# Performance work log

Hardware: AMD Instinct MI355X
Metric: run time of the kernel (lower is better)

Reference implementation:

```python
import jax, jax.numpy as jnp
import numpy as np

N_NODES = 8      # objects per graph (fixed in source)
N_AT = 16        # anchors/targets vocab: 8 colors + 8 markers
H = 128          # n_hidden
BS = 16384


def _mlp(x, W1, b1, W2, b2):
    # layers.fully_connected default activation is relu; second layer linear.
    # dropout is identity in eval mode.
    return jax.nn.relu(x @ W1 + b1) @ W2 + b2


def _edges_and_segments(bs):
    # static edge list: all ordered pairs (i,j), i != j, per graph, offset per batch
    ii, jj = np.meshgrid(np.arange(N_NODES), np.arange(N_NODES), indexing='ij')
    m = ii != jj
    base = np.stack([ii[m], jj[m]], axis=1)                      # [56, 2]
    offs = (np.arange(bs) * N_NODES)[:, None, None]
    edges = (base[None] + offs).reshape(-1, 2).astype(np.int32)  # [bs*56, 2]
    seg_ids = np.repeat(np.arange(bs), N_NODES).astype(np.int32) # [bs*8]
    return jnp.asarray(edges), jnp.asarray(seg_ids)


def setup_inputs() -> dict:
    key = jax.random.key(0)
    ks = jax.random.split(key, 14)

    anchors = jax.random.randint(ks[0], (BS,), 0, N_AT)
    n_jumps = jax.random.randint(ks[1], (BS,), 0, N_NODES)
    positions = jax.random.uniform(ks[2], (BS, N_NODES, 2), dtype=jnp.float32)
    colors = jax.random.randint(ks[3], (BS, N_NODES), 0, 8)
    markers = jax.random.randint(ks[4], (BS, N_NODES), 8, 16)  # markers live in [8,16)

    def lin(k, fan_in, fan_out):
        return jax.random.normal(k, (fan_in, fan_out), dtype=jnp.float32) / np.sqrt(fan_in)

    d_in = 2 + 8 + 8 + N_AT + N_NODES  # pos + color_oh + marker_oh + question(16+8) = 42
    z = lambda n: jnp.zeros((n,), jnp.float32)
    return {
        'anchors': anchors, 'n_jumps': n_jumps, 'positions': positions,
        'colors': colors, 'markers': markers,
        'pre_W1': lin(ks[5], d_in, H),     'pre_b1': z(H),
        'pre_W2': lin(ks[6], H, H),        'pre_b2': z(H),
        'msg_W1': lin(ks[7], 2 * H + 1, H),'msg_b1': z(H),
        'msg_W2': lin(ks[8], H, H),        'msg_b2': z(H),
        'post_W1': lin(ks[9], 2 * H, H),   'post_b1': z(H),
        'post_W2': lin(ks[10], H, H),      'post_b2': z(H),
        'out_W1': lin(ks[11], H, H),       'out_b1': z(H),
        'out_W2': lin(ks[12], H, N_AT),    'out_b2': z(N_AT),
    }


def reference(anchors, n_jumps, positions, colors, markers,
              pre_W1, pre_b1, pre_W2, pre_b2,
              msg_W1, msg_b1, msg_W2, msg_b2,
              post_W1, post_b1, post_W2, post_b2,
              out_W1, out_b1, out_W2, out_b2):
    bs = positions.shape[0]
    edges, seg_ids = _edges_and_segments(bs)
    n_total = bs * N_NODES

    col_oh = jax.nn.one_hot(colors, 8, dtype=jnp.float32).reshape(n_total, 8)
    mrk_oh = jax.nn.one_hot(markers - 8, 8, dtype=jnp.float32).reshape(n_total, 8)
    pos = positions.reshape(n_total, 2)

    # pairwise euclidean distance per edge -> [E, 1]
    dp = pos[edges[:, 0]] - pos[edges[:, 1]]
    dist = jnp.sqrt(jnp.sum(dp * dp, axis=1, keepdims=True))

    # question broadcast to every node of its graph
    q = jnp.concatenate([jax.nn.one_hot(anchors, N_AT, dtype=jnp.float32),
                         jax.nn.one_hot(n_jumps, N_NODES, dtype=jnp.float32)], axis=1)
    q = q[seg_ids]  # [bs*8, 24]

    x0 = _mlp(jnp.concatenate([pos, col_oh, mrk_oh, q], axis=1),
              pre_W1, pre_b1, pre_W2, pre_b2)  # [bs*8, H]

    # one message-passing step: gather -> MLP -> scatter(segment_sum on source idx)
    mi = jnp.concatenate([x0[edges[:, 0]], x0[edges[:, 1]], dist], axis=1)  # [E, 257]
    msgs = _mlp(mi, msg_W1, msg_b1, msg_W2, msg_b2)                          # [E, H]
    upd = jax.ops.segment_sum(msgs, edges[:, 0], num_segments=n_total)       # [bs*8, H]

    x = _mlp(jnp.concatenate([upd, x0], axis=1), post_W1, post_b1, post_W2, post_b2)

    logits = jax.ops.segment_sum(x, seg_ids, num_segments=bs)  # [bs, H]
    logits = _mlp(logits, out_W1, out_b1, out_W2, out_b2)      # [bs, 16]
    return logits
```

## Files before the change

kernel.cpp:

```cpp
#include <hip/hip_runtime.h>

#define LROW 136

typedef __bf16 bf16x8  __attribute__((ext_vector_type(8)));
typedef __bf16 bf16x4v __attribute__((ext_vector_type(4)));
typedef __bf16 bf16x2v __attribute__((ext_vector_type(2)));
typedef float  f32x4   __attribute__((ext_vector_type(4)));
typedef float  f32x2   __attribute__((ext_vector_type(2)));

#define MFMA16(a, b, c) __builtin_amdgcn_mfma_f32_16x16x32_bf16((a), (b), (c), 0, 0, 0)

__device__ __forceinline__ float bflo(unsigned v) { return __uint_as_float(v << 16); }
__device__ __forceinline__ float bfhi(unsigned v) { return __uint_as_float(v & 0xffff0000u); }

__device__ __forceinline__ unsigned short f2bf_u16(float f) {
  unsigned u = __float_as_uint(f);
  u += 0x7fffu + ((u >> 16) & 1u);
  return (unsigned short)(u >> 16);
}

__global__ void combine_weights(
    const float* __restrict__ pre_W2, const float* __restrict__ msg_W1,
    const float* __restrict__ msg_W2, const float* __restrict__ post_W1,
    const float* __restrict__ post_W2, const float* __restrict__ out_W1,
    const float* __restrict__ out_W2, const float* __restrict__ pre_b2,
    const float* __restrict__ msg_b1, const float* __restrict__ msg_b2,
    const float* __restrict__ post_b1, const float* __restrict__ post_b2,
    const float* __restrict__ out_b1,
    unsigned short* __restrict__ WabT, unsigned short* __restrict__ WdT,
    unsigned short* __restrict__ WcT, unsigned short* __restrict__ WoT,
    unsigned short* __restrict__ Wo2T, float* __restrict__ vecs)
{
  __shared__ float part[256];
  const int b = blockIdx.x;
  const int t = threadIdx.x;
  if (b < 320) {
    const int p  = b >> 6;
    const int kp = b & 63;
    const int k  = kp * 2 + (t >> 7);
    const int n  = t & 127;
    const float* L; const float* R; unsigned short* O;
    if (p == 0)      { L = pre_W2;  R = msg_W1;             O = WabT; }
    else if (p == 1) { L = pre_W2;  R = msg_W1 + 128*128;   O = WabT + 128*128; }
    else if (p == 2) { L = pre_W2;  R = post_W1 + 128*128;  O = WdT; }
    else if (p == 3) { L = msg_W2;  R = post_W1;            O = WcT; }
    else             { L = post_W2; R = out_W1;             O = WoT; }
    const float* Lr = L + k * 128;
    float a0 = 0.f, a1 = 0.f, a2 = 0.f, a3 = 0.f;
    #pragma unroll 8
    for (int m = 0; m < 128; m += 4) {
      a0 = fmaf(Lr[m + 0], R[(m + 0) * 128 + n], a0);
      a1 = fmaf(Lr[m + 1], R[(m + 1) * 128 + n], a1);
      a2 = fmaf(Lr[m + 2], R[(m + 2) * 128 + n], a2);
      a3 = fmaf(Lr[m + 3], R[(m + 3) * 128 + n], a3);
    }
    O[n * 128 + k] = f2bf_u16((a0 + a1) + (a2 + a3));
  } else if (b == 320) {
    for (int idx = t; idx < 16 * 128; idx += 256) {
      int o = idx >> 7, k = idx & 127;
      Wo2T[o * 128 + k] = f2bf_u16(out_W2[k * 16 + o]);
    }
    if (t < 128) vecs[t] = msg_W1[256 * 128 + t];
  } else {
    const int n = t & 127;
    const int h = t >> 7;
    float s = 0.f;
    if (b == 321) {
      #pragma unroll 8
      for (int m = h * 64; m < h * 64 + 64; ++m)
        s = fmaf(pre_b2[m], msg_W1[m * 128 + n] + msg_W1[(128 + m) * 128 + n], s);
    } else if (b == 322) {
      #pragma unroll 8
      for (int m = h * 64; m < h * 64 + 64; ++m) {
        s = fmaf(7.f * msg_b2[m], post_W1[m * 128 + n], s);
        s = fmaf(pre_b2[m], post_W1[(128 + m) * 128 + n], s);
      }
    } else {
      #pragma unroll 8
      for (int m = h * 64; m < h * 64 + 64; ++m)
        s = fmaf(8.f * post_b2[m], out_W1[m * 128 + n], s);
    }
    part[t] = s;
    __syncthreads();
    if (t < 128) {
      float r = part[t] + part[t + 128];
      if (b == 321)      vecs[128 + t] = r + msg_b1[t];
      else if (b == 322) vecs[256 + t] = r + post_b1[t];
      else               vecs[384 + t] = r + out_b1[t];
    }
  }
}

__global__ void __launch_bounds__(256, 4) rrn_main(
    const int* __restrict__ anchors, const int* __restrict__ n_jumps,
    const float* __restrict__ positions, const int* __restrict__ colors,
    const int* __restrict__ markers, const float* __restrict__ pre_W1,
    const float* __restrict__ pre_b1,
    const __bf16* __restrict__ WabT, const __bf16* __restrict__ WdT,
    const __bf16* __restrict__ WcT, const __bf16* __restrict__ WoT,
    const __bf16* __restrict__ Wo2T, const float* __restrict__ vecs,
    const float* __restrict__ out_b2, float* __restrict__ out)
{
  __shared__ __align__(16) char smem[38912];
  __bf16* Ab   = (__bf16*)(smem);
  float*  sW1s = (float*)(smem);
  float*  qrow = (float*)(smem + 9216);
  float*  posL = (float*)(smem + 13312);
  int*    cmk  = (int*)(smem + 13824);
  __bf16* h1   = (__bf16*)(smem + 17408);
  __bf16* Bb   = (__bf16*)(smem + 17408);
  __bf16* Sph  = (__bf16*)(smem + 17408);
  __bf16* hob  = (__bf16*)(smem + 21760);
  float*  dist = (float*)(smem + 34816);
  float*  vec  = (float*)(smem + 36864);

  const int tid  = threadIdx.x;
  const int lane = tid & 63;
  const int w    = tid >> 6;
  const int l15  = lane & 15;
  const int quad = lane >> 4;
  const int colw = w * 32;
  const int g0   = blockIdx.x * 8;
  const int n0   = blockIdx.x * 64;

  for (int i = tid; i < 18 * 128; i += 256) sW1s[i] = pre_W1[i];
  {
    const int n = tid & 127;
    for (int g = (tid >> 7); g < 8; g += 2) {
      int a = anchors[g0 + g], nj = n_jumps[g0 + g];
      qrow[g * 128 + n] = pre_b1[n] + pre_W1[(18 + a) * 128 + n]
                        + pre_W1[(34 + nj) * 128 + n];
    }
  }
  if (tid < 128) posL[tid] = positions[n0 * 2 + tid];
  else if (tid < 192) {
    int node = tid - 128;
    cmk[node] = colors[n0 + node] | ((markers[n0 + node] - 8) << 8);
  }
  for (int i = tid; i < 512; i += 256) {
    int g = i >> 6, ii = (i >> 3) & 7, jj = i & 7;
    const float* pa = positions + (n0 + g * 8 + ii) * 2;
    const float* pb = positions + (n0 + g * 8 + jj) * 2;
    float dx = pa[0] - pb[0], dy = pa[1] - pb[1];
    dist[i] = sqrtf(dx * dx + dy * dy);
  }
  for (int i = tid; i < 512; i += 256) vec[i] = vecs[i];
  __syncthreads();

  {
    const int p  = (tid & 63) * 2;
    const int rh = tid >> 6;
    const f32x2 z2 = {0.f, 0.f};
    const f32x2 wx = *(const f32x2*)&sW1s[p];
    const f32x2 wy = *(const f32x2*)&sW1s[128 + p];
    #pragma unroll 4
    for (int rr = 0; rr < 16; ++rr) {
      int r = rh * 16 + rr;
      float px = posL[r * 2], py = posL[r * 2 + 1];
      int cm = cmk[r];
      int c = cm & 255, mk = cm >> 8;
      f32x2 acc = *(const f32x2*)&qrow[(r >> 3) * 128 + p];
      acc += *(const f32x2*)&sW1s[(2 + c) * 128 + p];
      acc += *(const f32x2*)&sW1s[(10 + mk) * 128 + p];
      f32x2 px2 = {px, px}, py2 = {py, py};
      acc = __builtin_elementwise_fma(px2, wx, acc);
      acc = __builtin_elementwise_fma(py2, wy, acc);
      acc = __builtin_elementwise_max(acc, z2);
      bf16x2v o = { (__bf16)acc.x, (__bf16)acc.y };
      *(bf16x2v*)&h1[r * LROW + p] = o;
    }
  }
  __syncthreads();

  f32x4 acc1[4][4];
  {
    f32x4 zero = {0.f, 0.f, 0.f, 0.f};
    #pragma unroll
    for (int mt = 0; mt < 4; ++mt)
      #pragma unroll
      for (int nt = 0; nt < 4; ++nt) acc1[mt][nt] = zero;
  }
  #pragma unroll
  for (int kb = 0; kb < 128; kb += 32) {
    const int ko = kb + quad * 8;
    bf16x8 fa[4], fb[4];
    #pragma unroll
    for (int mt = 0; mt < 4; ++mt)
      fa[mt] = *(const bf16x8*)&h1[(mt * 16 + l15) * LROW + ko];
    fb[0] = *(const bf16x8*)&WabT[(colw + l15) * 128 + ko];
    fb[1] = *(const bf16x8*)&WabT[(colw + 16 + l15) * 128 + ko];
    fb[2] = *(const bf16x8*)&WabT[(128 + colw + l15) * 128 + ko];
    fb[3] = *(const bf16x8*)&WabT[(128 + colw + 16 + l15) * 128 + ko];
    #pragma unroll
    for (int mt = 0; mt < 4; ++mt)
      #pragma unroll
      for (int nt = 0; nt < 4; ++nt)
        acc1[mt][nt] = MFMA16(fa[mt], fb[nt], acc1[mt][nt]);
  }
  #pragma unroll
  for (int mt = 0; mt < 4; ++mt)
    #pragma unroll
    for (int nt = 0; nt < 2; ++nt) {
      int col = colw + nt * 16 + l15;
      #pragma unroll
      for (int r = 0; r < 4; ++r)
        Ab[(mt * 16 + quad * 4 + r) * LROW + col] = (__bf16)acc1[mt][nt][r];
    }

  f32x4 accD[4][2];
  {
    f32x4 zero = {0.f, 0.f, 0.f, 0.f};
    #pragma unroll
    for (int mt = 0; mt < 4; ++mt) { accD[mt][0] = zero; accD[mt][1] = zero; }
  }
  #pragma unroll
  for (int kb = 0; kb < 128; kb += 32) {
    const int ko = kb + quad * 8;
    bf16x8 fa[4], fd[2];
    #pragma unroll
    for (int mt = 0; mt < 4; ++mt)
      fa[mt] = *(const bf16x8*)&h1[(mt * 16 + l15) * LROW + ko];
    fd[0] = *(const bf16x8*)&WdT[(colw + l15) * 128 + ko];
    fd[1] = *(const bf16x8*)&WdT[(colw + 16 + l15) * 128 + ko];
    #pragma unroll
    for (int mt = 0; mt < 4; ++mt) {
      accD[mt][0] = MFMA16(fa[mt], fd[0], accD[mt][0]);
      accD[mt][1] = MFMA16(fa[mt], fd[1], accD[mt][1]);
    }
  }
  __syncthreads();
  #pragma unroll
  for (int mt = 0; mt < 4; ++mt)
    #pragma unroll
    for (int nt = 2; nt < 4; ++nt) {
      int col = colw + (nt - 2) * 16 + l15;
      #pragma unroll
      for (int r = 0; r < 4; ++r)
        Bb[(mt * 16 + quad * 4 + r) * LROW + col] = (__bf16)acc1[mt][nt][r];
    }
  __syncthreads();

  {
    const int g   = tid >> 5;
    const int nb4 = (tid & 31) * 4;
    const f32x2 w0 = *(const f32x2*)&vec[nb4];
    const f32x2 w1 = *(const f32x2*)&vec[nb4 + 2];
    const f32x2 c0 = *(const f32x2*)&vec[128 + nb4];
    const f32x2 c1 = *(const f32x2*)&vec[128 + nb4 + 2];
    const f32x2 z2 = {0.f, 0.f};
    f32x2 B0[8], B1[8];
    #pragma unroll
    for (int j = 0; j < 8; ++j) {
      uint2 vb = *(const uint2*)&Bb[(g * 8 + j) * LROW + nb4];
      B0[j].x = bflo(vb.x); B0[j].y = bfhi(vb.x);
      B1[j].x = bflo(vb.y); B1[j].y = bfhi(vb.y);
    }
    #pragma unroll
    for (int i = 0; i < 8; ++i) {
      uint2 va = *(const uint2*)&Ab[(g * 8 + i) * LROW + nb4];
      f32x2 a0; a0.x = bflo(va.x); a0.y = bfhi(va.x); a0 += c0;
      f32x2 a1; a1.x = bflo(va.y); a1.y = bfhi(va.y); a1 += c1;
      f32x2 s0 = z2, s1 = z2;
      #pragma unroll
      for (int j = 0; j < 8; ++j) {
        if (j == i) continue;
        float d = dist[g * 64 + i * 8 + j];
        f32x2 d2 = {d, d};
        f32x2 t0 = __builtin_elementwise_fma(d2, w0, B0[j]) + a0;
        f32x2 t1 = __builtin_elementwise_fma(d2, w1, B1[j]) + a1;
        t0 = __builtin_elementwise_max(t0, z2);
        t1 = __builtin_elementwise_max(t1, z2);
        s0 += t0; s1 += t1;
      }
      bf16x4v o = { (__bf16)s0.x, (__bf16)s0.y, (__bf16)s1.x, (__bf16)s1.y };
      *(bf16x4v*)&Ab[(g * 8 + i) * LROW + nb4] = o;
    }
  }
  __syncthreads();

  {
    const __bf16* Sb = Ab;
    #pragma unroll
    for (int kb = 0; kb < 128; kb += 32) {
      const int ko = kb + quad * 8;
      bf16x8 fa[4], fc[2];
      #pragma unroll
      for (int mt = 0; mt < 4; ++mt)
        fa[mt] = *(const bf16x8*)&Sb[(mt * 16 + l15) * LROW + ko];
      fc[0] = *(const bf16x8*)&WcT[(colw + l15) * 128 + ko];
      fc[1] = *(const bf16x8*)&WcT[(colw + 16 + l15) * 128 + ko];
      #pragma unroll
      for (int mt = 0; mt < 4; ++mt) {
        accD[mt][0] = MFMA16(fa[mt], fc[0], accD[mt][0]);
        accD[mt][1] = MFMA16(fa[mt], fc[1], accD[mt][1]);
      }
    }
    #pragma unroll
    for (int mt = 0; mt < 4; ++mt)
      #pragma unroll
      for (int dt = 0; dt < 2; ++dt) {
        int col = colw + dt * 16 + l15;
        float cp = vec[256 + col];
        f32x4 a = accD[mt][dt];
        float s = fmaxf(a[0] + cp, 0.f) + fmaxf(a[1] + cp, 0.f)
                + fmaxf(a[2] + cp, 0.f) + fmaxf(a[3] + cp, 0.f);
        s += __shfl_xor(s, 16);
        int grow = mt * 2 + (lane >= 32 ? 1 : 0);
        if ((lane & 31) < 16) Sph[grow * LROW + col] = (__bf16)s;
        else                  Sph[(8 + grow) * LROW + col] = (__bf16)0.f;
      }
  }
  __syncthreads();

  {
    f32x4 acco[2];
    f32x4 zero = {0.f, 0.f, 0.f, 0.f};
    acco[0] = zero; acco[1] = zero;
    #pragma unroll
    for (int kb = 0; kb < 128; kb += 32) {
      const int ko = kb + quad * 8;
      bf16x8 fa = *(const bf16x8*)&Sph[l15 * LROW + ko];
      bf16x8 fb0 = *(const bf16x8*)&WoT[(colw + l15) * 128 + ko];
      bf16x8 fb1 = *(const bf16x8*)&WoT[(colw + 16 + l15) * 128 + ko];
      acco[0] = MFMA16(fa, fb0, acco[0]);
      acco[1] = MFMA16(fa, fb1, acco[1]);
    }
    #pragma unroll
    for (int dt = 0; dt < 2; ++dt) {
      int col = colw + dt * 16 + l15;
      float co = vec[384 + col];
      #pragma unroll
      for (int r = 0; r < 4; ++r)
        hob[(quad * 4 + r) * LROW + col] = (__bf16)fmaxf(acco[dt][r] + co, 0.f);
    }
  }
  __syncthreads();

  if (w == 0) {
    f32x4 accf = {0.f, 0.f, 0.f, 0.f};
    #pragma unroll
    for (int kb = 0; kb < 128; kb += 32) {
      const int ko = kb + quad * 8;
      bf16x8 fa  = *(const bf16x8*)&hob[l15 * LROW + ko];
      bf16x8 fbv = *(const bf16x8*)&Wo2T[l15 * 128 + ko];
      accf = MFMA16(fa, fbv, accf);
    }
    if (quad < 2) {
      float b2 = out_b2[l15];
      #pragma unroll
      for (int r = 0; r < 4; ++r) {
        int row = quad * 4 + r;
        out[(g0 + row) * 16 + l15] = accf[r] + b2;
      }
    }
  }
}

extern "C" void kernel_launch(void* const* d_in, const int* in_sizes, int n_in,
                              void* d_out, int out_size, void* d_ws, size_t ws_size,
                              hipStream_t stream) {
  const int*   anchors   = (const int*)d_in[0];
  const int*   n_jumps   = (const int*)d_in[1];
  const float* positions = (const float*)d_in[2];
  const int*   colors    = (const int*)d_in[3];
  const int*   markers   = (const int*)d_in[4];
  const float* pre_W1  = (const float*)d_in[5];
  const float* pre_b1  = (const float*)d_in[6];
  const float* pre_W2  = (const float*)d_in[7];
  const float* pre_b2  = (const float*)d_in[8];
  const float* msg_W1  = (const float*)d_in[9];
  const float* msg_b1  = (const float*)d_in[10];
  const float* msg_W2  = (const float*)d_in[11];
  const float* msg_b2  = (const float*)d_in[12];
  const float* post_W1 = (const float*)d_in[13];
  const float* post_b1 = (const float*)d_in[14];
  const float* post_W2 = (const float*)d_in[15];
  const float* post_b2 = (const float*)d_in[16];
  const float* out_W1  = (const float*)d_in[17];
  const float* out_b1  = (const float*)d_in[18];
  const float* out_W2  = (const float*)d_in[19];
  const float* out_b2  = (const float*)d_in[20];

  char* ws = (char*)d_ws;
  unsigned short* WabT = (unsigned short*)(ws);
  unsigned short* WdT  = (unsigned short*)(ws + 65536);
  unsigned short* WcT  = (unsigned short*)(ws + 98304);
  unsigned short* WoT  = (unsigned short*)(ws + 131072);
  unsigned short* Wo2T = (unsigned short*)(ws + 163840);
  float*          vecs = (float*)(ws + 167936);

  const int BS = in_sizes[0];

  combine_weights<<<324, 256, 0, stream>>>(
      pre_W2, msg_W1, msg_W2, post_W1, post_W2, out_W1, out_W2,
      pre_b2, msg_b1, msg_b2, post_b1, post_b2, out_b1,
      WabT, WdT, WcT, WoT, Wo2T, vecs);

  rrn_main<<<BS / 8, 256, 0, stream>>>(
      anchors, n_jumps, positions, colors, markers, pre_W1, pre_b1,
      (const __bf16*)WabT, (const __bf16*)WdT, (const __bf16*)WcT,
      (const __bf16*)WoT, (const __bf16*)Wo2T, vecs, out_b2, (float*)d_out);
}
```

Baseline: 156.0 us.

## Halve graphs per block and shrink shared memory to raise occupancy

```diff
diff --git a/kernel.cpp b/kernel.cpp
--- a/kernel.cpp
+++ b/kernel.cpp
@@ -91,7 +91,7 @@
   }
 }
 
-__global__ void __launch_bounds__(256, 4) rrn_main(
+__global__ void __launch_bounds__(256, 6) rrn_main(
     const int* __restrict__ anchors, const int* __restrict__ n_jumps,
     const float* __restrict__ positions, const int* __restrict__ colors,
     const int* __restrict__ markers, const float* __restrict__ pre_W1,
@@ -101,18 +101,18 @@
     const __bf16* __restrict__ Wo2T, const float* __restrict__ vecs,
     const float* __restrict__ out_b2, float* __restrict__ out)
 {
-  __shared__ __align__(16) char smem[38912];
-  __bf16* Ab   = (__bf16*)(smem);
-  float*  sW1s = (float*)(smem);
-  float*  qrow = (float*)(smem + 9216);
-  float*  posL = (float*)(smem + 13312);
-  int*    cmk  = (int*)(smem + 13824);
-  __bf16* h1   = (__bf16*)(smem + 17408);
-  __bf16* Bb   = (__bf16*)(smem + 17408);
-  __bf16* Sph  = (__bf16*)(smem + 17408);
-  __bf16* hob  = (__bf16*)(smem + 21760);
-  float*  dist = (float*)(smem + 34816);
-  float*  vec  = (float*)(smem + 36864);
+  __shared__ __align__(16) char smem[20480];
+  float*  vec  = (float*)(smem);
+  float*  dist = (float*)(smem + 2048);
+  __bf16* Ab   = (__bf16*)(smem + 3072);
+  __bf16* sW1b = (__bf16*)(smem + 3072);
+  float*  qrow = (float*)(smem + 7680);
+  float*  posL = (float*)(smem + 9728);
+  short*  cmk  = (short*)(smem + 9984);
+  __bf16* h1   = (__bf16*)(smem + 11776);
+  __bf16* Bb   = (__bf16*)(smem + 11776);
+  __bf16* Sph  = (__bf16*)(smem + 11776);
+  __bf16* hob  = (__bf16*)(smem + 16128);
 
   const int tid  = threadIdx.x;
   const int lane = tid & 63;
@@ -120,48 +120,51 @@
   const int l15  = lane & 15;
   const int quad = lane >> 4;
   const int colw = w * 32;
-  const int g0   = blockIdx.x * 8;
-  const int n0   = blockIdx.x * 64;
-
-  for (int i = tid; i < 18 * 128; i += 256) sW1s[i] = pre_W1[i];
+  const int g0   = blockIdx.x * 4;
+  const int n0   = blockIdx.x * 32;
+
+  for (int i = tid; i < 18 * 128; i += 256) sW1b[i] = (__bf16)pre_W1[i];
   {
     const int n = tid & 127;
-    for (int g = (tid >> 7); g < 8; g += 2) {
+    for (int g = (tid >> 7); g < 4; g += 2) {
       int a = anchors[g0 + g], nj = n_jumps[g0 + g];
       qrow[g * 128 + n] = pre_b1[n] + pre_W1[(18 + a) * 128 + n]
                         + pre_W1[(34 + nj) * 128 + n];
     }
   }
-  if (tid < 128) posL[tid] = positions[n0 * 2 + tid];
-  else if (tid < 192) {
-    int node = tid - 128;
-    cmk[node] = colors[n0 + node] | ((markers[n0 + node] - 8) << 8);
-  }
-  for (int i = tid; i < 512; i += 256) {
-    int g = i >> 6, ii = (i >> 3) & 7, jj = i & 7;
+  if (tid < 64) posL[tid] = positions[n0 * 2 + tid];
+  else if (tid < 96) {
+    int node = tid - 64;
+    cmk[node] = (short)(colors[n0 + node] | ((markers[n0 + node] - 8) << 8));
+  }
+  {
+    int g = tid >> 6, ii = (tid >> 3) & 7, jj = tid & 7;
     const float* pa = positions + (n0 + g * 8 + ii) * 2;
     const float* pb = positions + (n0 + g * 8 + jj) * 2;
     float dx = pa[0] - pb[0], dy = pa[1] - pb[1];
-    dist[i] = sqrtf(dx * dx + dy * dy);
+    dist[tid] = sqrtf(dx * dx + dy * dy);
   }
   for (int i = tid; i < 512; i += 256) vec[i] = vecs[i];
   __syncthreads();
 
   {
-    const int p  = (tid & 63) * 2;
-    const int rh = tid >> 6;
+    const int p = lane * 2;
     const f32x2 z2 = {0.f, 0.f};
-    const f32x2 wx = *(const f32x2*)&sW1s[p];
-    const f32x2 wy = *(const f32x2*)&sW1s[128 + p];
-    #pragma unroll 4
-    for (int rr = 0; rr < 16; ++rr) {
-      int r = rh * 16 + rr;
+    unsigned vx = *(const unsigned*)&sW1b[p];
+    unsigned vy = *(const unsigned*)&sW1b[128 + p];
+    const f32x2 wx = {bflo(vx), bfhi(vx)};
+    const f32x2 wy = {bflo(vy), bfhi(vy)};
+    #pragma unroll
+    for (int rr = 0; rr < 8; ++rr) {
+      int r = w * 8 + rr;
       float px = posL[r * 2], py = posL[r * 2 + 1];
       int cm = cmk[r];
       int c = cm & 255, mk = cm >> 8;
       f32x2 acc = *(const f32x2*)&qrow[(r >> 3) * 128 + p];
-      acc += *(const f32x2*)&sW1s[(2 + c) * 128 + p];
-      acc += *(const f32x2*)&sW1s[(10 + mk) * 128 + p];
+      unsigned vc = *(const unsigned*)&sW1b[(2 + c) * 128 + p];
+      unsigned vm = *(const unsigned*)&sW1b[(10 + mk) * 128 + p];
+      f32x2 t = {bflo(vc) + bflo(vm), bfhi(vc) + bfhi(vm)};
+      acc += t;
       f32x2 px2 = {px, px}, py2 = {py, py};
       acc = __builtin_elementwise_fma(px2, wx, acc);
       acc = __builtin_elementwise_fma(py2, wy, acc);
@@ -172,33 +175,32 @@
   }
   __syncthreads();
 
-  f32x4 acc1[4][4];
+  f32x4 acc1[2][4];
   {
     f32x4 zero = {0.f, 0.f, 0.f, 0.f};
     #pragma unroll
-    for (int mt = 0; mt < 4; ++mt)
+    for (int mt = 0; mt < 2; ++mt)
       #pragma unroll
       for (int nt = 0; nt < 4; ++nt) acc1[mt][nt] = zero;
   }
   #pragma unroll
   for (int kb = 0; kb < 128; kb += 32) {
     const int ko = kb + quad * 8;
-    bf16x8 fa[4], fb[4];
-    #pragma unroll
-    for (int mt = 0; mt < 4; ++mt)
-      fa[mt] = *(const bf16x8*)&h1[(mt * 16 + l15) * LROW + ko];
+    bf16x8 fa[2], fb[4];
+    fa[0] = *(const bf16x8*)&h1[(l15) * LROW + ko];
+    fa[1] = *(const bf16x8*)&h1[(16 + l15) * LROW + ko];
     fb[0] = *(const bf16x8*)&WabT[(colw + l15) * 128 + ko];
     fb[1] = *(const bf16x8*)&WabT[(colw + 16 + l15) * 128 + ko];
     fb[2] = *(const bf16x8*)&WabT[(128 + colw + l15) * 128 + ko];
     fb[3] = *(const bf16x8*)&WabT[(128 + colw + 16 + l15) * 128 + ko];
     #pragma unroll
-    for (int mt = 0; mt < 4; ++mt)
+    for (int mt = 0; mt < 2; ++mt)
       #pragma unroll
       for (int nt = 0; nt < 4; ++nt)
         acc1[mt][nt] = MFMA16(fa[mt], fb[nt], acc1[mt][nt]);
   }
   #pragma unroll
-  for (int mt = 0; mt < 4; ++mt)
+  for (int mt = 0; mt < 2; ++mt)
     #pragma unroll
     for (int nt = 0; nt < 2; ++nt) {
       int col = colw + nt * 16 + l15;
@@ -207,30 +209,28 @@
         Ab[(mt * 16 + quad * 4 + r) * LROW + col] = (__bf16)acc1[mt][nt][r];
     }
 
-  f32x4 accD[4][2];
+  f32x4 accD[2][2];
   {
     f32x4 zero = {0.f, 0.f, 0.f, 0.f};
-    #pragma unroll
-    for (int mt = 0; mt < 4; ++mt) { accD[mt][0] = zero; accD[mt][1] = zero; }
+    accD[0][0] = zero; accD[0][1] = zero; accD[1][0] = zero; accD[1][1] = zero;
   }
   #pragma unroll
   for (int kb = 0; kb < 128; kb += 32) {
     const int ko = kb + quad * 8;
-    bf16x8 fa[4], fd[2];
-    #pragma unroll
-    for (int mt = 0; mt < 4; ++mt)
-      fa[mt] = *(const bf16x8*)&h1[(mt * 16 + l15) * LROW + ko];
+    bf16x8 fa[2], fd[2];
+    fa[0] = *(const bf16x8*)&h1[(l15) * LROW + ko];
+    fa[1] = *(const bf16x8*)&h1[(16 + l15) * LROW + ko];
     fd[0] = *(const bf16x8*)&WdT[(colw + l15) * 128 + ko];
     fd[1] = *(const bf16x8*)&WdT[(colw + 16 + l15) * 128 + ko];
     #pragma unroll
-    for (int mt = 0; mt < 4; ++mt) {
+    for (int mt = 0; mt < 2; ++mt) {
       accD[mt][0] = MFMA16(fa[mt], fd[0], accD[mt][0]);
       accD[mt][1] = MFMA16(fa[mt], fd[1], accD[mt][1]);
     }
   }
   __syncthreads();
   #pragma unroll
-  for (int mt = 0; mt < 4; ++mt)
+  for (int mt = 0; mt < 2; ++mt)
     #pragma unroll
     for (int nt = 2; nt < 4; ++nt) {
       int col = colw + (nt - 2) * 16 + l15;
@@ -241,62 +241,59 @@
   __syncthreads();
 
   {
-    const int g   = tid >> 5;
-    const int nb4 = (tid & 31) * 4;
-    const f32x2 w0 = *(const f32x2*)&vec[nb4];
-    const f32x2 w1 = *(const f32x2*)&vec[nb4 + 2];
-    const f32x2 c0 = *(const f32x2*)&vec[128 + nb4];
-    const f32x2 c1 = *(const f32x2*)&vec[128 + nb4 + 2];
+    const int g   = w;
+    const int nb2 = lane * 2;
+    const f32x2 w0 = *(const f32x2*)&vec[nb2];
+    const f32x2 c0 = *(const f32x2*)&vec[128 + nb2];
     const f32x2 z2 = {0.f, 0.f};
-    f32x2 B0[8], B1[8];
+    f32x2 B0[8];
     #pragma unroll
     for (int j = 0; j < 8; ++j) {
-      uint2 vb = *(const uint2*)&Bb[(g * 8 + j) * LROW + nb4];
-      B0[j].x = bflo(vb.x); B0[j].y = bfhi(vb.x);
-      B1[j].x = bflo(vb.y); B1[j].y = bfhi(vb.y);
+      unsigned vb = *(const unsigned*)&Bb[(g * 8 + j) * LROW + nb2];
+      B0[j].x = bflo(vb); B0[j].y = bfhi(vb);
     }
     #pragma unroll
     for (int i = 0; i < 8; ++i) {
-      uint2 va = *(const uint2*)&Ab[(g * 8 + i) * LROW + nb4];
-      f32x2 a0; a0.x = bflo(va.x); a0.y = bfhi(va.x); a0 += c0;
-      f32x2 a1; a1.x = bflo(va.y); a1.y = bfhi(va.y); a1 += c1;
-      f32x2 s0 = z2, s1 = z2;
+      unsigned va = *(const unsigned*)&Ab[(g * 8 + i) * LROW + nb2];
+      f32x2 a0 = {bflo(va), bfhi(va)};
+      a0 += c0;
+      f32x2 s0 = z2;
       #pragma unroll
       for (int j = 0; j < 8; ++j) {
         if (j == i) continue;
         float d = dist[g * 64 + i * 8 + j];
         f32x2 d2 = {d, d};
         f32x2 t0 = __builtin_elementwise_fma(d2, w0, B0[j]) + a0;
-        f32x2 t1 = __builtin_elementwise_fma(d2, w1, B1[j]) + a1;
         t0 = __builtin_elementwise_max(t0, z2);
-        t1 = __builtin_elementwise_max(t1, z2);
-        s0 += t0; s1 += t1;
+        s0 += t0;
       }
-      bf16x4v o = { (__bf16)s0.x, (__bf16)s0.y, (__bf16)s1.x, (__bf16)s1.y };
-      *(bf16x4v*)&Ab[(g * 8 + i) * LROW + nb4] = o;
-    }
-  }
-  __syncthreads();
-
-  {
+      bf16x2v o = { (__bf16)s0.x, (__bf16)s0.y };
+      *(bf16x2v*)&Ab[(g * 8 + i) * LROW + nb2] = o;
+    }
+  }
+  __syncthreads();
+
+  {
+    unsigned* zp = (unsigned*)(Sph + 4 * LROW);
+    for (int i = tid; i < (12 * LROW) / 2; i += 256) zp[i] = 0u;
+
     const __bf16* Sb = Ab;
     #pragma unroll
     for (int kb = 0; kb < 128; kb += 32) {
       const int ko = kb + quad * 8;
-      bf16x8 fa[4], fc[2];
-      #pragma unroll
-      for (int mt = 0; mt < 4; ++mt)
-        fa[mt] = *(const bf16x8*)&Sb[(mt * 16 + l15) * LROW + ko];
+      bf16x8 fa[2], fc[2];
+      fa[0] = *(const bf16x8*)&Sb[(l15) * LROW + ko];
+      fa[1] = *(const bf16x8*)&Sb[(16 + l15) * LROW + ko];
       fc[0] = *(const bf16x8*)&WcT[(colw + l15) * 128 + ko];
       fc[1] = *(const bf16x8*)&WcT[(colw + 16 + l15) * 128 + ko];
       #pragma unroll
-      for (int mt = 0; mt < 4; ++mt) {
+      for (int mt = 0; mt < 2; ++mt) {
         accD[mt][0] = MFMA16(fa[mt], fc[0], accD[mt][0]);
         accD[mt][1] = MFMA16(fa[mt], fc[1], accD[mt][1]);
       }
     }
     #pragma unroll
-    for (int mt = 0; mt < 4; ++mt)
+    for (int mt = 0; mt < 2; ++mt)
       #pragma unroll
       for (int dt = 0; dt < 2; ++dt) {
         int col = colw + dt * 16 + l15;
@@ -307,7 +304,6 @@
         s += __shfl_xor(s, 16);
         int grow = mt * 2 + (lane >= 32 ? 1 : 0);
         if ((lane & 31) < 16) Sph[grow * LROW + col] = (__bf16)s;
-        else                  Sph[(8 + grow) * LROW + col] = (__bf16)0.f;
       }
   }
   __syncthreads();
@@ -345,13 +341,11 @@
       bf16x8 fbv = *(const bf16x8*)&Wo2T[l15 * 128 + ko];
       accf = MFMA16(fa, fbv, accf);
     }
-    if (quad < 2) {
+    if (quad == 0) {
       float b2 = out_b2[l15];
       #pragma unroll
-      for (int r = 0; r < 4; ++r) {
-        int row = quad * 4 + r;
-        out[(g0 + row) * 16 + l15] = accf[r] + b2;
-      }
+      for (int r = 0; r < 4; ++r)
+        out[(g0 + r) * 16 + l15] = accf[r] + b2;
     }
   }
 }
@@ -396,7 +390,7 @@
       pre_b2, msg_b1, msg_b2, post_b1, post_b2, out_b1,
       WabT, WdT, WcT, WoT, Wo2T, vecs);
 
-  rrn_main<<<BS / 8, 256, 0, stream>>>(
+  rrn_main<<<BS / 4, 256, 0, stream>>>(
       anchors, n_jumps, positions, colors, markers, pre_W1, pre_b1,
       (const __bf16*)WabT, (const __bf16*)WdT, (const __bf16*)WcT,
       (const __bf16*)WoT, (const __bf16*)Wo2T, vecs, out_b2, (float*)d_out);
```

New measurement: 191.7 us. 1.23x slower.
